# Optimization experiments

Measured on AMD Instinct MI355X. Metric: run time of the kernel, lower is better.

Reference implementation:

```python
import jax, jax.numpy as jnp
import numpy as np

SELF_DIM = 6   # self_state_dim
HID = 50       # lstm_hidden_dim


def setup_inputs() -> dict:
    key = jax.random.key(0)
    ks = jax.random.split(key, 16)
    B, N, D = 8192, 64, 13  # batch, num humans, joint-state length

    def w(k, shape):
        # kaiming-ish init, stored as [in, out] so forward is x @ W + b
        return jax.random.normal(k, shape, jnp.float32) / jnp.sqrt(jnp.float32(shape[0]))

    z = lambda n: jnp.zeros((n,), jnp.float32)
    return {
        "state": jax.random.normal(ks[0], (B, N, D), jnp.float32),
        # mlp1: 13 -> 150 -> 100, last_relu=True
        "mlp1_w1": w(ks[1], (13, 150)),  "mlp1_b1": z(150),
        "mlp1_w2": w(ks[2], (150, 100)), "mlp1_b2": z(100),
        # attention: 200 -> 100 -> 100 -> 1 (no relu on last)
        "attn_w1": w(ks[3], (200, 100)), "attn_b1": z(100),
        "attn_w2": w(ks[4], (100, 100)), "attn_b2": z(100),
        "attn_w3": w(ks[5], (100, 1)),   "attn_b3": z(1),
        # LSTM(input=7, hidden=50), torch gate order i,f,g,o
        "lstm_wih": w(ks[6], (7, 4 * HID)),
        "lstm_whh": w(ks[7], (HID, 4 * HID)),
        "lstm_bih": z(4 * HID), "lstm_bhh": z(4 * HID),
        # mlp: 56 -> 150 -> 100 -> 100 -> 1
        "mlp_w1": w(ks[8], (SELF_DIM + HID, 150)), "mlp_b1": z(150),
        "mlp_w2": w(ks[9], (150, 100)),            "mlp_b2": z(100),
        "mlp_w3": w(ks[10], (100, 100)),           "mlp_b3": z(100),
        "mlp_w4": w(ks[11], (100, 1)),             "mlp_b4": z(1),
    }


def reference(state, mlp1_w1, mlp1_b1, mlp1_w2, mlp1_b2,
              attn_w1, attn_b1, attn_w2, attn_b2, attn_w3, attn_b3,
              lstm_wih, lstm_whh, lstm_bih, lstm_bhh,
              mlp_w1, mlp_b1, mlp_w2, mlp_b2, mlp_w3, mlp_b3, mlp_w4, mlp_b4):
    relu = jax.nn.relu
    B, N, D = state.shape
    self_state = state[:, 0, :SELF_DIM]      # [B, 6]
    human_state = state[:, :, SELF_DIM:]     # [B, N, 7]

    # mlp1 over all B*N per-human joint-state rows (last_relu=True)
    flat = state.reshape(B * N, D)
    m1 = relu(relu(flat @ mlp1_w1 + mlp1_b1) @ mlp1_w2 + mlp1_b2)   # [B*N, 100]

    # mean-pooled global state, broadcast back per human, concat, attention score
    gdim = m1.shape[-1]
    global_state = jnp.mean(m1.reshape(B, N, gdim), axis=1, keepdims=True)
    global_state = jnp.broadcast_to(global_state, (B, N, gdim)).reshape(B * N, gdim)
    a_in = jnp.concatenate([m1, global_state], axis=1)               # [B*N, 200]
    scores = (relu(relu(a_in @ attn_w1 + attn_b1) @ attn_w2 + attn_b2) @ attn_w3 + attn_b3)
    scores = scores.reshape(B, N)
    # NOTE: in the original torch code `scores` only feed `rerank_human_state`,
    # which is never consumed (dead code) -- the LSTM runs on the UNSORTED
    # human_state. We keep the score computation for fidelity; the per-sample
    # argsort/gather is dropped since it does not affect the output.

    # LSTM over the N humans (batch_first in torch, h0=c0=0)
    xs = jnp.transpose(human_state, (1, 0, 2))   # [N, B, 7]
    h0 = jnp.zeros((B, HID), state.dtype)

    def step(carry, x_t):
        h, c = carry
        gates = x_t @ lstm_wih + h @ lstm_whh + lstm_bih + lstm_bhh  # [B, 4H]
        i, f, g, o = jnp.split(gates, 4, axis=-1)
        c = jax.nn.sigmoid(f) * c + jax.nn.sigmoid(i) * jnp.tanh(g)
        h = jax.nn.sigmoid(o) * jnp.tanh(c)
        return (h, c), None

    (hn, _cn), _ = jax.lax.scan(step, (h0, h0), xs)

    # value head on [self_state, h_n]
    joint = jnp.concatenate([self_state, hn], axis=1)   # [B, 56]
    x = relu(joint @ mlp_w1 + mlp_b1)
    x = relu(x @ mlp_w2 + mlp_b2)
    x = relu(x @ mlp_w3 + mlp_b3)
    value = x @ mlp_w4 + mlp_b4                          # [B, 1]
    return value
```

## Files before the change

### kernel.cpp

```cpp
#include <hip/hip_runtime.h>

typedef __attribute__((ext_vector_type(8))) short short8;
typedef __attribute__((ext_vector_type(4))) float f32x4;
union frag_u { short8 v; unsigned short u[8]; };

__device__ __forceinline__ float bf2f(unsigned short b) {
  unsigned int u = ((unsigned int)b) << 16;
  float f; __builtin_memcpy(&f, &u, 4); return f;
}
__device__ __forceinline__ unsigned short f2bf(float f) {
  unsigned int u; __builtin_memcpy(&u, &f, 4);
  return (unsigned short)((u + 0x7FFFu + ((u >> 16) & 1u)) >> 16);
}
__device__ __forceinline__ unsigned short hi_of(float f) { return f2bf(f); }
__device__ __forceinline__ unsigned short lo_of(float f) {
  unsigned short h = f2bf(f); return f2bf(f - bf2f(h));
}
__device__ __forceinline__ float sigm(float x) {
  return __builtin_amdgcn_rcpf(1.f + __expf(-x));
}
__device__ __forceinline__ float tanh_(float x) {
  return 1.f - 2.f * __builtin_amdgcn_rcpf(1.f + __expf(2.f * x));
}

__global__ void detect_dtype_kernel(const unsigned short* s, int* flag) {
  int i = threadIdx.x;
  unsigned short v = s[2 * i];
  int e = (v >> 7) & 0xFF;
  unsigned long long m = __ballot(e < 100 || e > 140);
  if (i == 0) *flag = (__popcll(m) >= 16) ? 1 : 0;
}

template <int AS, typename GetB, typename GetW>
__device__ __forceinline__ void mfma_layer(const unsigned short* sA, float* sG,
    int wave, int col, int quad, int kc_n, int ntiles, int N, GetB getb, GetW getw)
{
  for (int tile = wave; tile < ntiles; tile += 16) {
    int n = tile * 16 + col;
    float b = (n < N) ? getb(n) : 0.f;
    f32x4 acc = {b, b, b, b};
    for (int kc = 0; kc < kc_n; ++kc) {
      short8 a = *(const short8*)&sA[col * AS + kc * 32 + quad * 8];
      frag_u w;
      #pragma unroll
      for (int j = 0; j < 8; ++j) {
        int k = kc * 32 + quad * 8 + j;
        w.u[j] = (n < N) ? getw(k, n) : (unsigned short)0;
      }
      acc = __builtin_amdgcn_mfma_f32_16x16x32_bf16(a, w.v, acc, 0, 0, 0);
    }
    *(f32x4*)&sG[n * 20 + quad * 4] = acc;
  }
}

template <int AS, bool LO>
__device__ __forceinline__ void relu_fill(const float* sG, unsigned short* sA,
                                          int tid, int N, int loOff, int Kpad) {
  for (int idx = tid; idx < 16 * Kpad; idx += 1024) {
    int m = idx & 15, n = idx >> 4;
    unsigned short v = 0;
    if (n < N) {
      v = f2bf(fmaxf(sG[n * 20 + m], 0.f));
    } else if (LO && n >= loOff && n < loOff + N) {
      float x = fmaxf(sG[(n - loOff) * 20 + m], 0.f);
      v = lo_of(x);
    }
    sA[m * AS + n] = v;
  }
}

template <bool F32>
__global__ __launch_bounds__(1024, 8) void value_net_kernel(
    const void* state_, const void* wih_, const void* whh_,
    const void* bih_, const void* bhh_,
    const void* w1_, const void* b1_, const void* w2_, const void* b2_,
    const void* w3_, const void* b3_, const void* w4_, const void* b4_,
    void* out_, const int* flag)
{
  if (flag && *flag != (F32 ? 1 : 0)) return;

  constexpr int AS = F32 ? 328 : 168;
  constexpr int KC = F32 ? 6 : 4;

  __shared__ __align__(16) unsigned short sA[2][16 * AS];
  __shared__ __align__(16) float sG[208 * 20];

  const unsigned short* st16 = (const unsigned short*)state_;
  const float*          stf  = (const float*)state_;

  const int tid  = threadIdx.x;
  const int wave = tid >> 6;
  const int lane = tid & 63;
  const int col  = lane & 15;
  const int quad = lane >> 4;
  const int r0   = blockIdx.x * 16;

  {
    unsigned int* a32 = (unsigned int*)&sA[0][0];
    constexpr int ZT = 16 * AS;
    #pragma unroll
    for (int i = 0; i < (ZT + 1023) / 1024; ++i) {
      int idx = tid + i * 1024;
      if (idx < ZT) a32[idx] = 0;
    }
  }

  auto W_lstm = [&](int k, int n) -> unsigned short {
    if constexpr (!F32) {
      const unsigned short* wih = (const unsigned short*)wih_;
      const unsigned short* whh = (const unsigned short*)whh_;
      if (k < 7)   return wih[k * 200 + n];
      if (k < 57)  return whh[(k - 7) * 200 + n];
      if (k < 107) return whh[(k - 57) * 200 + n];
      return (unsigned short)0;
    } else {
      const float* wih = (const float*)wih_;
      const float* whh = (const float*)whh_;
      if (k < 7)   return hi_of(wih[k * 200 + n]);
      if (k < 14)  return hi_of(wih[(k - 7) * 200 + n]);
      if (k < 21)  return lo_of(wih[(k - 14) * 200 + n]);
      if (k < 71)  return hi_of(whh[(k - 21) * 200 + n]);
      if (k < 121) return hi_of(whh[(k - 71) * 200 + n]);
      if (k < 171) return lo_of(whh[(k - 121) * 200 + n]);
      return (unsigned short)0;
    }
  };
  auto ldf = [&](const void* p, int i) -> float {
    if constexpr (F32) return ((const float*)p)[i];
    else               return bf2f(((const unsigned short*)p)[i]);
  };

  const bool hasTile = (wave < 13);
  frag_u wf[KC];
  float  wb = 0.f;
  if (hasTile) {
    int nn = wave * 16 + col;
    int no = (nn < 200) ? ((nn & 3) * 50 + (nn >> 2)) : 0;
    #pragma unroll
    for (int kc = 0; kc < KC; ++kc) {
      #pragma unroll
      for (int j = 0; j < 8; ++j) {
        int k = kc * 32 + quad * 8 + j;
        wf[kc].u[j] = (nn < 200) ? W_lstm(k, no) : (unsigned short)0;
      }
    }
    wb = (nn < 200) ? (ldf(bih_, no) + ldf(bhh_, no)) : 0.f;
  }

  const int  u_   = wave * 4 + quad;
  const bool iact = hasTile && (u_ < 50);
  float c_ = 0.f, hf = 0.f;

  const bool isx = (tid >= 832) && (tid < 944);
  const int  xm = (tid - 832) / 7, xd = (tid - 832) - ((tid - 832) / 7) * 7;
  auto xgidx = [&](int t) -> size_t { return (size_t)(r0 + xm) * 832 + t * 13 + 6 + xd; };
  auto xwrite = [&](unsigned short* sAw, float fv, unsigned short bv) {
    if constexpr (!F32) { sAw[xm * AS + xd] = bv; }
    else {
      unsigned short h = f2bf(fv);
      sAw[xm * AS + xd] = h; sAw[xm * AS + 14 + xd] = h;
      sAw[xm * AS + 7 + xd] = f2bf(fv - bf2f(h));
    }
  };
  unsigned short xv16 = 0; float xvf = 0.f;

  __syncthreads();
  if (isx) {
    if constexpr (!F32) { xwrite(&sA[0][0], 0.f, st16[xgidx(0)]); xv16 = st16[xgidx(1)]; }
    else                { xwrite(&sA[0][0], stf[xgidx(0)], 0);    xvf  = stf[xgidx(1)]; }
  }
  __syncthreads();

  for (int t = 0; t < 64; ++t) {
    const unsigned short* sAr = &sA[t & 1][0];
    unsigned short*       sAw = &sA[(t & 1) ^ 1][0];

    if (hasTile) {
      short8 a[KC];
      #pragma unroll
      for (int kc = 0; kc < KC; ++kc)
        a[kc] = *(const short8*)&sAr[col * AS + kc * 32 + quad * 8];
      f32x4 acc = {wb, wb, wb, wb};
      #pragma unroll
      for (int kc = 0; kc < KC; ++kc)
        acc = __builtin_amdgcn_mfma_f32_16x16x32_bf16(a[kc], wf[kc].v, acc, 0, 0, 0);
      *(f32x4*)&sG[(wave * 16 + col) * 20 + quad * 4] = acc;

      if (iact) {
        int nb = (wave * 16 + quad * 4);
        float gi = sG[(nb + 0) * 20 + col];
        float gf = sG[(nb + 1) * 20 + col];
        float gg = sG[(nb + 2) * 20 + col];
        float go = sG[(nb + 3) * 20 + col];
        float cc = sigm(gf) * c_ + sigm(gi) * tanh_(gg);
        c_ = cc;
        float h = sigm(go) * tanh_(cc);
        if (t < 63) {
          unsigned short hb = f2bf(h);
          unsigned short hl = f2bf(h - bf2f(hb));
          if constexpr (!F32) {
            sAw[col * AS + 7 + u_] = hb; sAw[col * AS + 57 + u_] = hl;
          } else {
            sAw[col * AS + 21 + u_] = hb; sAw[col * AS + 121 + u_] = hb;
            sAw[col * AS + 71 + u_] = hl;
          }
        } else hf = h;
      }
    } else if (isx && t < 63) {
      if constexpr (!F32) xwrite(sAw, 0.f, xv16); else xwrite(sAw, xvf, 0);
      if (t < 62) { if constexpr (!F32) xv16 = st16[xgidx(t + 2)]; else xvf = stf[xgidx(t + 2)]; }
    }
    __syncthreads();
  }

  unsigned short* sA0 = &sA[0][0];
  {
    unsigned int* a32 = (unsigned int*)sA0;
    #pragma unroll
    for (int i = 0; i < (16 * AS / 2 + 1023) / 1024; ++i) {
      int idx = tid + i * 1024;
      if (idx < 16 * AS / 2) a32[idx] = 0;
    }
  }
  __syncthreads();
  if (iact) {
    unsigned short hb = f2bf(hf);
    unsigned short hl = f2bf(hf - bf2f(hb));
    sA0[col * AS + 6 + u_] = hb;
    if constexpr (!F32) sA0[col * AS + 56 + u_] = hl; else sA0[col * AS + 62 + u_] = hl;
  }
  if (tid < 96) {
    int m = tid / 6, d = tid - (tid / 6) * 6;
    if constexpr (!F32) sA0[m * AS + d] = st16[(size_t)(r0 + m) * 832 + d];
    else {
      float f = stf[(size_t)(r0 + m) * 832 + d];
      sA0[m * AS + d] = hi_of(f); sA0[m * AS + 56 + d] = lo_of(f);
    }
  }
  __syncthreads();

  mfma_layer<AS>(sA0, sG, wave, col, quad, 4, 10, 150,
    [&](int n) { return ldf(b1_, n); },
    [&](int k, int n) -> unsigned short {
      if constexpr (!F32) {
        const unsigned short* w1 = (const unsigned short*)w1_;
        if (k < 56)  return w1[k * 150 + n];
        if (k < 106) return w1[(k - 50) * 150 + n];
        return (unsigned short)0;
      } else {
        const float* w1 = (const float*)w1_;
        if (k < 56)  return hi_of(w1[k * 150 + n]);
        if (k < 112) return hi_of(w1[(k - 56) * 150 + n]);
        return (unsigned short)0;
      }
    });
  __syncthreads();
  if constexpr (!F32) relu_fill<AS, false>(sG, sA0, tid, 150, 160, 160);
  else                relu_fill<AS, true >(sG, sA0, tid, 150, 150, 320);
  __syncthreads();

  mfma_layer<AS>(sA0, sG, wave, col, quad, F32 ? 10 : 5, 7, 100,
    [&](int n) { return ldf(b2_, n); },
    [&](int k, int n) -> unsigned short {
      if constexpr (!F32) {
        const unsigned short* w2 = (const unsigned short*)w2_;
        return (k < 150) ? w2[k * 100 + n] : (unsigned short)0;
      } else {
        const float* w2 = (const float*)w2_;
        if (k < 150) return hi_of(w2[k * 100 + n]);
        if (k < 300) return hi_of(w2[(k - 150) * 100 + n]);
        return (unsigned short)0;
      }
    });
  __syncthreads();
  if constexpr (!F32) relu_fill<AS, false>(sG, sA0, tid, 100, 128, 128);
  else                relu_fill<AS, true >(sG, sA0, tid, 100, 100, 224);
  __syncthreads();

  mfma_layer<AS>(sA0, sG, wave, col, quad, F32 ? 7 : 4, 7, 100,
    [&](int n) { return ldf(b3_, n); },
    [&](int k, int n) -> unsigned short {
      if constexpr (!F32) {
        const unsigned short* w3 = (const unsigned short*)w3_;
        return (k < 100) ? w3[k * 100 + n] : (unsigned short)0;
      } else {
        const float* w3 = (const float*)w3_;
        if (k < 100) return hi_of(w3[k * 100 + n]);
        if (k < 200) return hi_of(w3[(k - 100) * 100 + n]);
        return (unsigned short)0;
      }
    });
  __syncthreads();

  if (tid < 256) {
    int m = tid >> 4, j0 = tid & 15;
    float s = 0.f;
    for (int j = j0; j < 100; j += 16)
      s += fmaxf(sG[j * 20 + m], 0.f) * ldf(w4_, j);
    s += __shfl_xor(s, 8); s += __shfl_xor(s, 4);
    s += __shfl_xor(s, 2); s += __shfl_xor(s, 1);
    if (j0 == 0) {
      float v = s + ldf(b4_, 0);
      if constexpr (!F32) ((unsigned short*)out_)[r0 + m] = f2bf(v);
      else                ((float*)out_)[r0 + m] = v;
    }
  }
}

extern "C" void kernel_launch(void* const* d_in, const int* in_sizes, int n_in,
                              void* d_out, int out_size, void* d_ws, size_t ws_size,
                              hipStream_t stream) {
  (void)n_in; (void)out_size;
  const void* state = d_in[0];
  const void* wih = d_in[11]; const void* whh = d_in[12];
  const void* bih = d_in[13]; const void* bhh = d_in[14];
  const void* w1  = d_in[15]; const void* b1  = d_in[16];
  const void* w2  = d_in[17]; const void* b2  = d_in[18];
  const void* w3  = d_in[19]; const void* b3  = d_in[20];
  const void* w4  = d_in[21]; const void* b4  = d_in[22];

  const long long F32B  = 8192LL * 64 * 13 * 4;
  const long long BF16B = 8192LL * 64 * 13 * 2;
  long long sz = in_sizes ? (long long)in_sizes[0] : -1;

  if (sz == F32B) {
    value_net_kernel<true><<<dim3(512), dim3(1024), 0, stream>>>(
        state, wih, whh, bih, bhh, w1, b1, w2, b2, w3, b3, w4, b4, d_out,
        (const int*)nullptr);
  } else if (sz == BF16B) {
    value_net_kernel<false><<<dim3(512), dim3(1024), 0, stream>>>(
        state, wih, whh, bih, bhh, w1, b1, w2, b2, w3, b3, w4, b4, d_out,
        (const int*)nullptr);
  } else if (ws_size >= sizeof(int)) {
    int* flag = (int*)d_ws;
    detect_dtype_kernel<<<dim3(1), dim3(64), 0, stream>>>(
        (const unsigned short*)state, flag);
    value_net_kernel<false><<<dim3(512), dim3(1024), 0, stream>>>(
        state, wih, whh, bih, bhh, w1, b1, w2, b2, w3, b3, w4, b4, d_out, flag);
    value_net_kernel<true><<<dim3(512), dim3(1024), 0, stream>>>(
        state, wih, whh, bih, bhh, w1, b1, w2, b2, w3, b3, w4, b4, d_out, flag);
  } else {
    value_net_kernel<false><<<dim3(512), dim3(1024), 0, stream>>>(
        state, wih, whh, bih, bhh, w1, b1, w2, b2, w3, b3, w4, b4, d_out,
        (const int*)nullptr);
  }
}
```

Baseline: 230.2 us.

## Preload LSTM inputs to LDS, fuse gate activations, pack hidden hi/lo writes

```diff
diff --git a/kernel.cpp b/kernel.cpp
--- a/kernel.cpp
+++ b/kernel.cpp
@@ -16,11 +16,23 @@
 __device__ __forceinline__ unsigned short lo_of(float f) {
   unsigned short h = f2bf(f); return f2bf(f - bf2f(h));
 }
-__device__ __forceinline__ float sigm(float x) {
-  return __builtin_amdgcn_rcpf(1.f + __expf(-x));
-}
-__device__ __forceinline__ float tanh_(float x) {
-  return 1.f - 2.f * __builtin_amdgcn_rcpf(1.f + __expf(2.f * x));
+
+__device__ __forceinline__ void lstm_act(float gi, float gf, float gg, float go,
+                                         float& c, float& h) {
+  gi = fminf(fmaxf(gi, -15.f), 15.f);
+  gf = fminf(fmaxf(gf, -15.f), 15.f);
+  gg = fminf(fmaxf(gg, -15.f), 15.f);
+  go = fminf(fmaxf(go, -15.f), 15.f);
+  float A = 1.f + __expf(-gf);
+  float B = 1.f + __expf(-gi);
+  float C = 1.f + __expf(2.f * gg);
+  float BC  = B * C;
+  float num = c * BC + A * (C - 2.f);
+  c = num * __builtin_amdgcn_rcpf(A * BC);
+  float D  = 1.f + __expf(-go);
+  float cl = fminf(fmaxf(c, -15.f), 15.f);
+  float E  = 1.f + __expf(2.f * cl);
+  h = (E - 2.f) * __builtin_amdgcn_rcpf(D * E);
 }
 
 __global__ void detect_dtype_kernel(const unsigned short* s, int* flag) {
@@ -84,6 +96,7 @@
 
   __shared__ __align__(16) unsigned short sA[2][16 * AS];
   __shared__ __align__(16) float sG[208 * 20];
+  __shared__ __align__(16) unsigned short sX[1024 * 8 * (F32 ? 2 : 1)];
 
   const unsigned short* st16 = (const unsigned short*)state_;
   const float*          stf  = (const float*)state_;
@@ -105,13 +118,31 @@
     }
   }
 
+  {
+    int r = tid >> 6, t = tid & 63;
+    size_t g = (size_t)(r0 + r) * 832 + (size_t)t * 13 + 6;
+    int base = (t * 16 + r) * 8;
+    if constexpr (!F32) {
+      #pragma unroll
+      for (int d = 0; d < 7; ++d) sX[base + d] = st16[g + d];
+    } else {
+      #pragma unroll
+      for (int d = 0; d < 7; ++d) {
+        float f = stf[g + d];
+        unsigned short h = f2bf(f);
+        sX[2 * (base + d) + 0] = h;
+        sX[2 * (base + d) + 1] = f2bf(f - bf2f(h));
+      }
+    }
+  }
+
   auto W_lstm = [&](int k, int n) -> unsigned short {
     if constexpr (!F32) {
       const unsigned short* wih = (const unsigned short*)wih_;
       const unsigned short* whh = (const unsigned short*)whh_;
       if (k < 7)   return wih[k * 200 + n];
-      if (k < 57)  return whh[(k - 7) * 200 + n];
-      if (k < 107) return whh[(k - 57) * 200 + n];
+      if (k < 8)   return (unsigned short)0;
+      if (k < 108) return whh[((k - 8) >> 1) * 200 + n];
       return (unsigned short)0;
     } else {
       const float* wih = (const float*)wih_;
@@ -119,9 +150,9 @@
       if (k < 7)   return hi_of(wih[k * 200 + n]);
       if (k < 14)  return hi_of(wih[(k - 7) * 200 + n]);
       if (k < 21)  return lo_of(wih[(k - 14) * 200 + n]);
-      if (k < 71)  return hi_of(whh[(k - 21) * 200 + n]);
-      if (k < 121) return hi_of(whh[(k - 71) * 200 + n]);
-      if (k < 171) return lo_of(whh[(k - 121) * 200 + n]);
+      if (k < 22)  return (unsigned short)0;
+      if (k < 122) return hi_of(whh[((k - 22) >> 1) * 200 + n]);
+      if (k < 172) return lo_of(whh[(k - 122) * 200 + n]);
       return (unsigned short)0;
     }
   };
@@ -153,22 +184,19 @@
 
   const bool isx = (tid >= 832) && (tid < 944);
   const int  xm = (tid - 832) / 7, xd = (tid - 832) - ((tid - 832) / 7) * 7;
-  auto xgidx = [&](int t) -> size_t { return (size_t)(r0 + xm) * 832 + t * 13 + 6 + xd; };
-  auto xwrite = [&](unsigned short* sAw, float fv, unsigned short bv) {
-    if constexpr (!F32) { sAw[xm * AS + xd] = bv; }
-    else {
-      unsigned short h = f2bf(fv);
+  auto xfeed = [&](unsigned short* sAw, int t) {
+    int base = (t * 16 + xm) * 8 + xd;
+    if constexpr (!F32) {
+      sAw[xm * AS + xd] = sX[base];
+    } else {
+      unsigned short h = sX[2 * base + 0], l = sX[2 * base + 1];
       sAw[xm * AS + xd] = h; sAw[xm * AS + 14 + xd] = h;
-      sAw[xm * AS + 7 + xd] = f2bf(fv - bf2f(h));
+      sAw[xm * AS + 7 + xd] = l;
     }
   };
-  unsigned short xv16 = 0; float xvf = 0.f;
-
-  __syncthreads();
-  if (isx) {
-    if constexpr (!F32) { xwrite(&sA[0][0], 0.f, st16[xgidx(0)]); xv16 = st16[xgidx(1)]; }
-    else                { xwrite(&sA[0][0], stf[xgidx(0)], 0);    xvf  = stf[xgidx(1)]; }
-  }
+
+  __syncthreads();
+  if (isx) xfeed(&sA[0][0], 0);
   __syncthreads();
 
   for (int t = 0; t < 64; ++t) {
@@ -187,28 +215,27 @@
       *(f32x4*)&sG[(wave * 16 + col) * 20 + quad * 4] = acc;
 
       if (iact) {
-        int nb = (wave * 16 + quad * 4);
+        int nb = wave * 16 + quad * 4;
         float gi = sG[(nb + 0) * 20 + col];
         float gf = sG[(nb + 1) * 20 + col];
         float gg = sG[(nb + 2) * 20 + col];
         float go = sG[(nb + 3) * 20 + col];
-        float cc = sigm(gf) * c_ + sigm(gi) * tanh_(gg);
-        c_ = cc;
-        float h = sigm(go) * tanh_(cc);
+        float h;
+        lstm_act(gi, gf, gg, go, c_, h);
         if (t < 63) {
           unsigned short hb = f2bf(h);
           unsigned short hl = f2bf(h - bf2f(hb));
+          unsigned int pack = (unsigned int)hb | ((unsigned int)hl << 16);
           if constexpr (!F32) {
-            sAw[col * AS + 7 + u_] = hb; sAw[col * AS + 57 + u_] = hl;
+            *(unsigned int*)&sAw[col * AS + 8 + 2 * u_] = pack;
           } else {
-            sAw[col * AS + 21 + u_] = hb; sAw[col * AS + 121 + u_] = hb;
-            sAw[col * AS + 71 + u_] = hl;
+            *(unsigned int*)&sAw[col * AS + 22 + 2 * u_] = pack;
+            sAw[col * AS + 122 + u_] = hb;
           }
         } else hf = h;
       }
     } else if (isx && t < 63) {
-      if constexpr (!F32) xwrite(sAw, 0.f, xv16); else xwrite(sAw, xvf, 0);
-      if (t < 62) { if constexpr (!F32) xv16 = st16[xgidx(t + 2)]; else xvf = stf[xgidx(t + 2)]; }
+      xfeed(sAw, t + 1);
     }
     __syncthreads();
   }
```

New measurement: 235.5 us. +2.3%, slower.
